# Optimization experiments

Hardware: AMD Instinct MI355X
Metric: run time of the kernel (lower is better)

## Reference

```python
import jax, jax.numpy as jnp
import numpy as np

NUM_LAYERS = 6
DIM = 512
VOCAB = 50257
HEADS = 8
EXPERTS = 8
TOPK = 2
LN_EPS = 1e-5


def setup_inputs() -> dict:
    key = jax.random.key(0)
    ks = jax.random.split(key, 9)
    d, L, E = DIM, NUM_LAYERS, EXPERTS
    return {
        'input_ids': jax.random.randint(ks[0], (2, 1024), 0, VOCAB),
        'embed': jax.random.normal(ks[1], (VOCAB, d), dtype=jnp.float32) * 0.02,
        'qkv_w': jax.random.normal(ks[2], (L, 3 * d, d), dtype=jnp.float32) * 0.02,
        'out_w': jax.random.normal(ks[3], (L, d, d), dtype=jnp.float32) * 0.02,
        'router_w': jax.random.normal(ks[4], (L, E, d), dtype=jnp.float32) * 0.02,
        'router_b': jnp.zeros((L, E), dtype=jnp.float32),
        'w1': jax.random.normal(ks[5], (L, E, 2 * d, d), dtype=jnp.float32) * 0.02,
        'b1': jnp.zeros((L, E, 2 * d), dtype=jnp.float32),
        'w2': jax.random.normal(ks[6], (L, E, d, 2 * d), dtype=jnp.float32) * 0.02,
        'b2': jnp.zeros((L, E, d), dtype=jnp.float32),
        'ln_g': jnp.ones((L, d), dtype=jnp.float32),
        'ln_b': jnp.zeros((L, d), dtype=jnp.float32),
        'head_w': jax.random.normal(ks[7], (VOCAB, d), dtype=jnp.float32) * 0.02,
    }


def _bit_weight(w):
    # BitNet 1.58b training-mode effective weight (STE forward value):
    # scale = mean|w| per output row; w_eff = round(w/scale).clip(-1,1) * scale
    scale = jnp.clip(jnp.mean(jnp.abs(w), axis=-1, keepdims=True), 1e-5, None)
    wq = jnp.clip(jnp.round(w / scale), -1.0, 1.0)
    w_ste = jax.lax.stop_gradient(wq - w) + w
    return w_ste * scale


def _layer_norm(x, g, b):
    mu = jnp.mean(x, axis=-1, keepdims=True)
    var = jnp.mean(jnp.square(x - mu), axis=-1, keepdims=True)
    return (x - mu) * jax.lax.rsqrt(var + LN_EPS) * g + b


def _attention(x, qkv_w, out_w):
    B, Lq, D = x.shape
    hd = D // HEADS
    qkv = (x @ qkv_w.T).reshape(B, Lq, 3, HEADS, hd).transpose(2, 0, 3, 1, 4)
    q, k, v = qkv[0], qkv[1], qkv[2]  # [B,H,L,hd]
    attn = jax.nn.softmax(jnp.einsum('bhqd,bhkd->bhqk', q, k) * hd ** -0.5, axis=-1)
    o = jnp.einsum('bhqk,bhkd->bhqd', attn, v).transpose(0, 2, 1, 3).reshape(B, Lq, D)
    return o @ out_w.T


def _moe(x, rw, rb, w1, b1, w2, b2, g, beta):
    B, Lq, D = x.shape
    N = B * Lq
    xf = x.reshape(N, D)
    probs = jax.nn.softmax(xf @ rw.T + rb, axis=-1)  # [N,E]
    vals, idx = jax.lax.top_k(probs, TOPK)
    vals = vals / (jnp.sum(vals, axis=-1, keepdims=True) + 1e-8)
    # combine weights: [N,E] (top-k indices are distinct, so sum == scatter)
    cw = jnp.sum(jax.nn.one_hot(idx, EXPERTS, dtype=xf.dtype) * vals[..., None], axis=1)
    we1 = _bit_weight(w1)  # [E,2D,D]
    we2 = _bit_weight(w2)  # [E,D,2D]
    h = jax.nn.gelu(jnp.einsum('nd,efd->enf', xf, we1) + b1[:, None, :], approximate=False)
    y = jnp.einsum('enf,edf->end', h, we2) + b2[:, None, :]  # [E,N,D]
    out = jnp.einsum('ne,end->nd', cw, y)
    return _layer_norm(out + xf, g, beta).reshape(B, Lq, D)


def reference(input_ids, embed, qkv_w, out_w, router_w, router_b, w1, b1, w2, b2, ln_g, ln_b, head_w):
    x = embed[input_ids]  # [B,L,D]
    for l in range(NUM_LAYERS):
        x = x + _attention(x, qkv_w[l], out_w[l])
        x = _moe(x, router_w[l], router_b[l], w1[l], b1[l], w2[l], b2[l], ln_g[l], ln_b[l])
    return x @ head_w.T  # logits [B,L,V]
```

## Files before the change

### kernel.cpp

```cpp
#include <hip/hip_runtime.h>
#include <math.h>
#include <stdint.h>

#define NLAYER 6
#define DIMD 512
#define HEADS 8
#define HD 64
#define EXPERTS 8
#define SEQ 1024
#define NTOK 2048
#define FF 1024
#define VOCABN 50257
#define HROWS 50432

typedef __bf16 bf16;
typedef __bf16 bf16x8 __attribute__((ext_vector_type(8)));
typedef __bf16 bf16x4 __attribute__((ext_vector_type(4)));
typedef float f32x4 __attribute__((ext_vector_type(4)));

__device__ __forceinline__ void gl_lds16(const void* g, void* l) {
  __builtin_amdgcn_global_load_lds(
      (const __attribute__((address_space(1))) void*)(uintptr_t)g,
      (__attribute__((address_space(3))) void*)(uintptr_t)l, 16, 0, 0);
}

#define LDSW(row, kg) (((row) * 32) + ((((kg) ^ (((row) >> 1) & 3))) << 3))

__global__ __launch_bounds__(256) void k_mfma_gemm(
    const bf16* __restrict__ A0, const bf16* __restrict__ A1,
    const bf16* __restrict__ B0, const bf16* __restrict__ B1,
    float* __restrict__ Cf, bf16* __restrict__ Cb0, bf16* __restrict__ Cb1,
    bf16* __restrict__ Cb2, bf16* __restrict__ E0, bf16* __restrict__ E1,
    bf16* __restrict__ E2, int M, int N, int K,
    long sA, long sB, long sCf, long sCb,
    const float* __restrict__ colScale, int csStride,
    const float* __restrict__ bias, int biasStride,
    const float* __restrict__ residual, int act, int mode,
    const int* __restrict__ mLimit, const int* __restrict__ aperm,
    int outmode) {
  __shared__ __align__(16) bf16 As[2][128 * 32];
  __shared__ __align__(16) bf16 Bs[2][128 * 32];
  int tid = threadIdx.x;
  int z = blockIdx.z;
  int nwg = gridDim.x * gridDim.y;
  int flat = blockIdx.y * gridDim.x + blockIdx.x;
  int qq = nwg >> 3, rr = nwg & 7;
  int xcd = flat & 7, ii = flat >> 3;
  int swz = (xcd < rr ? xcd * (qq + 1) : rr * (qq + 1) + (xcd - rr) * qq) + ii;
  int m0 = (swz % gridDim.x) * 128, n0 = (swz / gridDim.x) * 128;
  if (mLimit && m0 >= mLimit[z]) return;
  int w = tid >> 6, lane = tid & 63;
  int wm = (w >> 1) * 64, wn = (w & 1) * 64;
  int r15 = lane & 15, kg = lane >> 4;

  int pa[3] = {0, 0, 0}, pb[3] = {0, 0, 0};
  int np = 1;
  if (mode == 3) {
    np = 2; pa[1] = 1;
  } else if (mode == 5) {
    np = 3;
    pa[1] = 0; pb[1] = 1; pa[2] = 1; pb[2] = 0;
  }

  f32x4 acc[4][4] = {};
  int srow = tid >> 2;
  int scol = (((tid & 3) ^ ((tid >> 3) & 3))) << 3;
  long arow0, arow1;
  if (aperm) {
    arow0 = aperm[z * 2048 + m0 + srow];
    arow1 = aperm[z * 2048 + m0 + 64 + srow];
  } else {
    arow0 = m0 + srow;
    arow1 = m0 + 64 + srow;
  }
  const bf16* PA[2] = {A0, A1};
  const bf16* PB[2] = {B0, B1};

  const int kIters = K / 32;
  const int nIter = np * kIters;
  int sp = 0, staged = 0;
  const bf16 *sa0, *sa1, *sb0, *sb1;
  auto resetPassPtrs = [&](int p) {
    const bf16* Az = PA[pa[p]] + (long)z * sA;
    const bf16* Bz = PB[pb[p]] + (long)z * sB;
    sa0 = Az + arow0 * K + scol;
    sa1 = Az + arow1 * K + scol;
    sb0 = Bz + (long)(n0 + srow) * K + scol;
    sb1 = Bz + (long)(n0 + 64 + srow) * K + scol;
  };
  resetPassPtrs(0);
  auto stage = [&](int buf) {
    gl_lds16(sa0, &As[buf][tid * 8]);
    gl_lds16(sa1, &As[buf][2048 + tid * 8]);
    gl_lds16(sb0, &Bs[buf][tid * 8]);
    gl_lds16(sb1, &Bs[buf][2048 + tid * 8]);
    sa0 += 32; sa1 += 32; sb0 += 32; sb1 += 32;
    if (++staged == kIters) {
      staged = 0;
      if (++sp < np) resetPassPtrs(sp);
    }
  };
  auto compute = [&](int buf) {
    bf16x8 af[4], bfr[4];
#pragma unroll
    for (int mi = 0; mi < 4; ++mi) {
      int rowA = wm + mi * 16 + r15;
      af[mi] = *(const bf16x8*)&As[buf][LDSW(rowA, kg)];
    }
#pragma unroll
    for (int ni = 0; ni < 4; ++ni) {
      int rowB = wn + ni * 16 + r15;
      bfr[ni] = *(const bf16x8*)&Bs[buf][LDSW(rowB, kg)];
    }
#pragma unroll
    for (int mi = 0; mi < 4; ++mi)
#pragma unroll
      for (int ni = 0; ni < 4; ++ni)
        acc[mi][ni] = __builtin_amdgcn_mfma_f32_16x16x32_bf16(
            af[mi], bfr[ni], acc[mi][ni], 0, 0, 0);
  };

  stage(0);
  stage(1);
#pragma unroll 1
  for (int it = 0; it < nIter - 2; ++it) {
    asm volatile("s_waitcnt vmcnt(4)" ::: "memory");
    __builtin_amdgcn_s_barrier();
    __builtin_amdgcn_sched_barrier(0);
    compute(it & 1);
    __builtin_amdgcn_s_barrier();
    stage(it & 1);
  }
  asm volatile("s_waitcnt vmcnt(4)" ::: "memory");
  __builtin_amdgcn_s_barrier();
  __builtin_amdgcn_sched_barrier(0);
  compute(nIter & 1);
  asm volatile("s_waitcnt vmcnt(0)" ::: "memory");
  __builtin_amdgcn_s_barrier();
  __builtin_amdgcn_sched_barrier(0);
  compute((nIter - 1) & 1);

#pragma unroll
  for (int mi = 0; mi < 4; ++mi) {
    int rbase = m0 + wm + mi * 16 + kg * 4;
#pragma unroll
    for (int ni = 0; ni < 4; ++ni) {
      int col = n0 + wn + ni * 16 + r15;
      if (col >= N) continue;
      float scl = colScale ? colScale[z * csStride + col] : 1.f;
      float bv = bias ? bias[z * biasStride + col] : 0.f;
#pragma unroll
      for (int reg = 0; reg < 4; ++reg) {
        int row = rbase + reg;
        float v = acc[mi][ni][reg] * scl + bv;
        if (act) v = 0.5f * v * (1.f + erff(v * 0.70710678118654752f));
        if (residual) v += residual[(long)row * N + col];
        if (outmode == 2) {
          int b = row >> 10, qt = row & 1023;
          if (n0 < 512) {
            float qv = v * 0.125f;
            int h = col >> 6, d = col & 63;
            long dst = ((long)(b * 8 + h)) * ((long)SEQ * HD) +
                       (long)qt * HD + d;
            bf16 h0 = (bf16)qv;
            Cb0[dst] = h0;
            Cb1[dst] = (bf16)(qv - (float)h0);
          } else if (n0 < 1024) {
            int c2 = col - 512;
            int h = c2 >> 6, d = c2 & 63;
            long dst = ((long)(b * 8 + h)) * ((long)SEQ * HD) +
                       (long)qt * HD + d;
            bf16 h0 = (bf16)v;
            Cb2[dst] = h0;
            E0[dst] = (bf16)(v - (float)h0);
          } else {
            int c2 = col - 1024;
            int h = c2 >> 6, d = c2 & 63;
            long dst = ((long)(b * 8 + h)) * ((long)HD * SEQ) +
                       (long)d * SEQ + qt;
            bf16 h0 = (bf16)v;
            E1[dst] = h0;
            E2[dst] = (bf16)(v - (float)h0);
          }
          continue;
        }
        if (Cf) Cf[z * sCf + (long)row * N + col] = v;
        if (Cb0) {
          long cib = z * sCb + (long)row * N + col;
          bf16 h0 = (bf16)v;
          Cb0[cib] = h0;
          if (Cb1) {
            float r = v - (float)h0;
            Cb1[cib] = (bf16)r;
          }
        }
      }
    }
  }
}

__global__ __launch_bounds__(256) void k_fattn(
    const bf16* __restrict__ q0b, const bf16* __restrict__ q1b,
    const bf16* __restrict__ k0b, const bf16* __restrict__ k1b,
    const bf16* __restrict__ vt0, const bf16* __restrict__ vt1,
    bf16* __restrict__ at0, bf16* __restrict__ at1) {
  __shared__ __align__(16) bf16 Ks[2][64 * 64];
  __shared__ __align__(16) bf16 Vs[2][64 * 64];
  __shared__ __align__(16) bf16 Ps[2][64 * 64];
  int tid = threadIdx.x;
  int bh = blockIdx.y;
  int q0 = blockIdx.x * 64;
  int w = tid >> 6, lane = tid & 63;
  int r15 = lane & 15, kg = lane >> 4;
  const long bhQK = (long)bh * SEQ * HD;
  const long bhV = (long)bh * HD * SEQ;

  bf16x8 qa0[2], qa1[2];
  {
    long qoff = bhQK + (long)(q0 + w * 16 + r15) * HD;
#pragma unroll
    for (int ks = 0; ks < 2; ++ks) {
      qa0[ks] = *(const bf16x8*)&q0b[qoff + ks * 32 + kg * 8];
      qa1[ks] = *(const bf16x8*)&q1b[qoff + ks * 32 + kg * 8];
    }
  }

  auto stageK = [&](int kt) {
#pragma unroll
    for (int i = 0; i < 2; ++i) {
      int L = tid + i * 256;
      int row = L >> 3, pc = L & 7;
      int gc = pc ^ (row & 7);
      long gsrc = bhQK + (long)(kt * 64 + row) * HD + gc * 8;
      gl_lds16(k0b + gsrc, &Ks[0][L * 8]);
      gl_lds16(k1b + gsrc, &Ks[1][L * 8]);
    }
  };
  auto stageV = [&](int kt) {
#pragma unroll
    for (int i = 0; i < 2; ++i) {
      int L = tid + i * 256;
      int row = L >> 3, pc = L & 7;
      int gc = pc ^ (row & 7);
      long gsrc = bhV + (long)row * SEQ + kt * 64 + gc * 8;
      gl_lds16(vt0 + gsrc, &Vs[0][L * 8]);
      gl_lds16(vt1 + gsrc, &Vs[1][L * 8]);
    }
  };
  auto computeS = [&](f32x4* sf) {
    __builtin_amdgcn_s_setprio(1);
#pragma unroll
    for (int kc = 0; kc < 4; ++kc) {
      f32x4 a = {};
      int rowB = kc * 16 + r15;
#pragma unroll
      for (int ks = 0; ks < 2; ++ks) {
        int pc = (ks * 4 + kg) ^ (rowB & 7);
        bf16x8 b0 = *(const bf16x8*)&Ks[0][rowB * 64 + pc * 8];
        bf16x8 b1 = *(const bf16x8*)&Ks[1][rowB * 64 + pc * 8];
        a = __builtin_amdgcn_mfma_f32_16x16x32_bf16(qa0[ks], b0, a, 0, 0, 0);
        a = __builtin_amdgcn_mfma_f32_16x16x32_bf16(qa0[ks], b1, a, 0, 0, 0);
        a = __builtin_amdgcn_mfma_f32_16x16x32_bf16(qa1[ks], b0, a, 0, 0, 0);
      }
      sf[kc] = a;
    }
    __builtin_amdgcn_s_setprio(0);
  };

  float m[4], l[4];
#pragma unroll
  for (int r = 0; r < 4; ++r) { m[r] = -1e30f; l[r] = 0.f; }
  f32x4 oacc[4] = {};

  for (int kt = 0; kt < SEQ / 64; ++kt) {
    stageK(kt);
    stageV(kt);
    __syncthreads();
    f32x4 sf[4];
    computeS(sf);
#pragma unroll
    for (int r = 0; r < 4; ++r) {
      float tm = sf[0][r];
#pragma unroll
      for (int kc = 1; kc < 4; ++kc) tm = fmaxf(tm, sf[kc][r]);
      tm = fmaxf(tm, __shfl_xor(tm, 1));
      tm = fmaxf(tm, __shfl_xor(tm, 2));
      tm = fmaxf(tm, __shfl_xor(tm, 4));
      tm = fmaxf(tm, __shfl_xor(tm, 8));
      float mn = fmaxf(m[r], tm);
      float corr = __expf(m[r] - mn);
      float s = 0.f;
#pragma unroll
      for (int kc = 0; kc < 4; ++kc) {
        float p = __expf(sf[kc][r] - mn);
        sf[kc][r] = p;
        s += p;
      }
      s += __shfl_xor(s, 1);
      s += __shfl_xor(s, 2);
      s += __shfl_xor(s, 4);
      s += __shfl_xor(s, 8);
      l[r] = l[r] * corr + s;
      m[r] = mn;
#pragma unroll
      for (int dg = 0; dg < 4; ++dg) oacc[dg][r] *= corr;
    }
#pragma unroll
    for (int kc = 0; kc < 4; ++kc) {
#pragma unroll
      for (int r = 0; r < 4; ++r) {
        float p = sf[kc][r];
        bf16 h0 = (bf16)p;
        bf16 h1 = (bf16)(p - (float)h0);
        int qrow = w * 16 + kg * 4 + r;
        int kcol = kc * 16 + r15;
        int pc = (kcol >> 3) ^ (qrow & 7);
        int addr = qrow * 64 + pc * 8 + (kcol & 7);
        Ps[0][addr] = h0;
        Ps[1][addr] = h1;
      }
    }
    bf16x8 pa0[2], pa1[2];
    int rowP = w * 16 + r15;
#pragma unroll
    for (int ks = 0; ks < 2; ++ks) {
      int pc = (ks * 4 + kg) ^ (rowP & 7);
      pa0[ks] = *(const bf16x8*)&Ps[0][rowP * 64 + pc * 8];
      pa1[ks] = *(const bf16x8*)&Ps[1][rowP * 64 + pc * 8];
    }
    __builtin_amdgcn_s_setprio(1);
#pragma unroll
    for (int dg = 0; dg < 4; ++dg) {
      int rowV = dg * 16 + r15;
#pragma unroll
      for (int ks = 0; ks < 2; ++ks) {
        int pc = (ks * 4 + kg) ^ (rowV & 7);
        bf16x8 v0 = *(const bf16x8*)&Vs[0][rowV * 64 + pc * 8];
        bf16x8 v1 = *(const bf16x8*)&Vs[1][rowV * 64 + pc * 8];
        oacc[dg] = __builtin_amdgcn_mfma_f32_16x16x32_bf16(pa0[ks], v0,
                                                           oacc[dg], 0, 0, 0);
        oacc[dg] = __builtin_amdgcn_mfma_f32_16x16x32_bf16(pa0[ks], v1,
                                                           oacc[dg], 0, 0, 0);
        oacc[dg] = __builtin_amdgcn_mfma_f32_16x16x32_bf16(pa1[ks], v0,
                                                           oacc[dg], 0, 0, 0);
      }
    }
    __builtin_amdgcn_s_setprio(0);
    __syncthreads();
  }

  float invl[4];
#pragma unroll
  for (int r = 0; r < 4; ++r) invl[r] = 1.f / l[r];

  int b = bh >> 3, h = bh & 7;
#pragma unroll
  for (int dg = 0; dg < 4; ++dg) {
#pragma unroll
    for (int r = 0; r < 4; ++r) {
      int qrow = q0 + w * 16 + kg * 4 + r;
      int d = dg * 16 + r15;
      long dst = ((long)(b * SEQ + qrow)) * DIMD + h * HD + d;
      float v = oacc[dg][r] * invl[r];
      bf16 h0 = (bf16)v;
      at0[dst] = h0;
      at1[dst] = (bf16)(v - (float)h0);
    }
  }
}

__global__ __launch_bounds__(512, 2) void k_hgemm(const bf16* __restrict__ A,
                                                  const bf16* __restrict__ Bt,
                                                  float* __restrict__ C,
                                                  int M, int N, int K) {
  __shared__ __align__(16) bf16 As[2][256 * 64];
  __shared__ __align__(16) bf16 Bs[2][256 * 64];
  int tid = threadIdx.x;
  int nwg = gridDim.x * gridDim.y;
  int flat = blockIdx.y * gridDim.x + blockIdx.x;
  int qq = nwg >> 3, rr = nwg & 7;
  int xcd = flat & 7, ii = flat >> 3;
  int swz = (xcd < rr ? xcd * (qq + 1) : rr * (qq + 1) + (xcd - rr) * qq) + ii;
  int m0 = (swz % gridDim.x) * 256, n0 = (swz / gridDim.x) * 256;
  int w = tid >> 6, lane = tid & 63;
  int wm = (w >> 2) * 128, wn = (w & 3) * 64;
  int r15 = lane & 15, kg = lane >> 4;

  auto stage = [&](int buf, int kt) {
#pragma unroll
    for (int j = 0; j < 4; ++j) {
      int L = tid + j * 512;
      int row = L >> 3, pc = L & 7;
      int gc = pc ^ (row & 7);
      gl_lds16(A + (long)(m0 + row) * K + kt * 64 + gc * 8, &As[buf][L * 8]);
      gl_lds16(Bt + (long)(n0 + row) * K + kt * 64 + gc * 8, &Bs[buf][L * 8]);
    }
  };

  f32x4 acc[8][4] = {};
  auto compute = [&](int buf) {
#pragma unroll
    for (int ks = 0; ks < 2; ++ks) {
      bf16x8 af[8], bf_[4];
#pragma unroll
      for (int mi = 0; mi < 8; ++mi) {
        int row = wm + mi * 16 + r15;
        af[mi] = *(const bf16x8*)
            &As[buf][row * 64 + ((((ks * 4 + kg) ^ (row & 7))) << 3)];
      }
#pragma unroll
      for (int ni = 0; ni < 4; ++ni) {
        int row = wn + ni * 16 + r15;
        bf_[ni] = *(const bf16x8*)
            &Bs[buf][row * 64 + ((((ks * 4 + kg) ^ (row & 7))) << 3)];
      }
#pragma unroll
      for (int mi = 0; mi < 8; ++mi)
#pragma unroll
        for (int ni = 0; ni < 4; ++ni)
          acc[mi][ni] = __builtin_amdgcn_mfma_f32_16x16x32_bf16(
              af[mi], bf_[ni], acc[mi][ni], 0, 0, 0);
    }
  };

  stage(0, 0);
  stage(1, 1);
#pragma unroll 1
  for (int t = 0; t < 6; ++t) {
    asm volatile("s_waitcnt vmcnt(8)" ::: "memory");
    __builtin_amdgcn_s_barrier();
    __builtin_amdgcn_sched_barrier(0);
    compute(t & 1);
    __builtin_amdgcn_s_barrier();
    stage(t & 1, t + 2);
  }
  asm volatile("s_waitcnt vmcnt(8)" ::: "memory");
  __builtin_amdgcn_s_barrier();
  __builtin_amdgcn_sched_barrier(0);
  compute(0);
  asm volatile("s_waitcnt vmcnt(0)" ::: "memory");
  __builtin_amdgcn_s_barrier();
  __builtin_amdgcn_sched_barrier(0);
  compute(1);

#pragma unroll
  for (int mi = 0; mi < 8; ++mi) {
    int rbase = m0 + wm + mi * 16 + kg * 4;
#pragma unroll
    for (int ni = 0; ni < 4; ++ni) {
      int col = n0 + wn + ni * 16 + r15;
      if (col >= N) continue;
#pragma unroll
      for (int reg = 0; reg < 4; ++reg)
        C[(long)(rbase + reg) * N + col] = acc[mi][ni][reg];
    }
  }
}

__global__ __launch_bounds__(256) void k_embed(const int* __restrict__ ids,
                                               const float* __restrict__ E,
                                               float* __restrict__ xf,
                                               bf16* __restrict__ x0,
                                               bf16* __restrict__ x1) {
  int i = blockIdx.x * 256 + threadIdx.x;
  if (i >= NTOK * DIMD) return;
  int n = i >> 9, d = i & 511;
  float v = E[(long)ids[n] * DIMD + d];
  xf[i] = v;
  bf16 b0 = (bf16)v;
  x0[i] = b0;
  x1[i] = (bf16)(v - (float)b0);
}

__global__ __launch_bounds__(256) void k_prepw(const float* __restrict__ qkv_w,
                                               const float* __restrict__ out_w,
                                               bf16* __restrict__ qw0a,
                                               bf16* __restrict__ qw1a,
                                               bf16* __restrict__ ow0a,
                                               bf16* __restrict__ ow1a) {
  int l = blockIdx.y;
  const long n8q = (long)3 * DIMD * DIMD / 8;
  long i = (long)blockIdx.x * 256 + threadIdx.x;
  const float* s;
  bf16 *d0, *d1;
  long j;
  if (i < n8q) {
    s = qkv_w + (long)l * 3 * DIMD * DIMD;
    d0 = qw0a + (long)l * 3 * DIMD * DIMD;
    d1 = qw1a + (long)l * 3 * DIMD * DIMD;
    j = i;
  } else {
    s = out_w + (long)l * DIMD * DIMD;
    d0 = ow0a + (long)l * DIMD * DIMD;
    d1 = ow1a + (long)l * DIMD * DIMD;
    j = i - n8q;
  }
  const float4* s4 = (const float4*)s;
  float4 a = s4[2 * j], b = s4[2 * j + 1];
  float vv[8] = {a.x, a.y, a.z, a.w, b.x, b.y, b.z, b.w};
  bf16x8 o0, o1;
#pragma unroll
  for (int k = 0; k < 8; ++k) {
    float v = vv[k];
    bf16 h0 = (bf16)v;
    o0[k] = h0;
    o1[k] = (bf16)(v - (float)h0);
  }
  ((bf16x8*)d0)[j] = o0;
  ((bf16x8*)d1)[j] = o1;
}

__global__ __launch_bounds__(256) void k_headconv(const float* __restrict__ s,
                                                  bf16* __restrict__ d) {
  long i = (long)blockIdx.x * 256 + threadIdx.x;
  long n8 = (long)HROWS * DIMD / 8;
  if (i >= n8) return;
  long row = i / (DIMD / 8);
  bf16x8 o;
  if (row < VOCABN) {
    const float4* s4 = (const float4*)s;
    float4 a = s4[2 * i], b = s4[2 * i + 1];
    o[0] = (bf16)a.x; o[1] = (bf16)a.y; o[2] = (bf16)a.z; o[3] = (bf16)a.w;
    o[4] = (bf16)b.x; o[5] = (bf16)b.y; o[6] = (bf16)b.z; o[7] = (bf16)b.w;
  } else {
    o = (bf16x8)(bf16)0.f;
  }
  ((bf16x8*)d)[i] = o;
}

__global__ __launch_bounds__(64) void k_router(const float* __restrict__ x,
                                               const float* __restrict__ rw,
                                               const float* __restrict__ rb,
                                               int* __restrict__ top2,
                                               float* __restrict__ v2) {
  int n = blockIdx.x;
  int t = threadIdx.x;
  int e = t >> 3, part = t & 7;
  __shared__ float red[64];
  const float* xr = x + (long)n * DIMD;
  const float* wr = rw + (long)e * DIMD;
  float d = 0.f;
  int c0 = part * 64;
#pragma unroll
  for (int c = 0; c < 64; c += 4) {
    float4 xv = *(const float4*)(xr + c0 + c);
    float4 wv = *(const float4*)(wr + c0 + c);
    d += xv.x * wv.x + xv.y * wv.y + xv.z * wv.z + xv.w * wv.w;
  }
  red[t] = d;
  __syncthreads();
  if (t < 8) {
    float logit = rb[t];
    for (int pp = 0; pp < 8; ++pp) logit += red[t * 8 + pp];
    red[t] = logit;
  }
  __syncthreads();
  if (t == 0) {
    float p2[8];
    float m = -1e30f;
    for (int i = 0; i < 8; ++i) m = fmaxf(m, red[i]);
    float s = 0.f;
    for (int i = 0; i < 8; ++i) { p2[i] = expf(red[i] - m); s += p2[i]; }
    for (int i = 0; i < 8; ++i) p2[i] /= s;
    int i1 = 0;
    for (int i = 1; i < 8; ++i) if (p2[i] > p2[i1]) i1 = i;
    int i2 = (i1 == 0) ? 1 : 0;
    for (int i = 0; i < 8; ++i) {
      if (i == i1 || i == i2) continue;
      if (p2[i] > p2[i2]) i2 = i;
    }
    float sum = p2[i1] + p2[i2] + 1e-8f;
    top2[2 * n] = i1;
    top2[2 * n + 1] = i2;
    v2[2 * n] = p2[i1] / sum;
    v2[2 * n + 1] = p2[i2] / sum;
  }
}

__global__ __launch_bounds__(256) void k_expcnt(const int* __restrict__ top2,
                                                int* __restrict__ perm,
                                                int* __restrict__ tokpos,
                                                int* __restrict__ cnt,
                                                bf16* __restrict__ zx0,
                                                bf16* __restrict__ zx1) {
  int e = blockIdx.x, t = threadIdx.x;
  if (e == 0) {
    for (int c = t; c < DIMD; c += 256) {
      zx0[c] = (bf16)0.f;
      zx1[c] = (bf16)0.f;
    }
  }
  __shared__ int sc[256];
  int fl[8];
  int f = 0;
#pragma unroll
  for (int j = 0; j < 8; ++j) {
    int n = t * 8 + j;
    int m = (top2[2 * n] == e || top2[2 * n + 1] == e) ? 1 : 0;
    fl[j] = m;
    f += m;
  }
  sc[t] = f;
  __syncthreads();
  for (int o = 1; o < 256; o <<= 1) {
    int v = (t >= o) ? sc[t - o] : 0;
    __syncthreads();
    sc[t] += v;
    __syncthreads();
  }
  int pos = sc[t] - f;
#pragma unroll
  for (int j = 0; j < 8; ++j) {
    if (fl[j]) {
      int n = t * 8 + j;
      perm[e * 2048 + pos] = n;
      int jj = (top2[2 * n] == e) ? 0 : 1;
      tokpos[2 * n + jj] = e * 2048 + pos;
      ++pos;
    }
  }
  int total = sc[255];
  int cpad = (total + 127) & ~127;
  for (int i = total + t; i < cpad; i += 256) perm[e * 2048 + i] = 2048;
  if (t == 0) cnt[e] = total;
}

__global__ __launch_bounds__(256) void k_bitw2(const float* __restrict__ w1,
                                               const float* __restrict__ w2,
                                               bf16* __restrict__ we1qa,
                                               float* __restrict__ s1a,
                                               bf16* __restrict__ we2qa,
                                               float* __restrict__ s2a) {
  int l = blockIdx.y;
  int blk = blockIdx.x;
  int t = threadIdx.x;
  const float* wr;
  bf16* outr;
  float* sOut;
  int cols;
  if (blk < EXPERTS * FF) {
    cols = DIMD;
    wr = w1 + (long)l * EXPERTS * FF * DIMD + (long)blk * cols;
    outr = we1qa + (long)l * EXPERTS * FF * DIMD + (long)blk * cols;
    sOut = s1a + (long)l * EXPERTS * FF + blk;
  } else {
    int row = blk - EXPERTS * FF;
    cols = FF;
    wr = w2 + (long)l * EXPERTS * DIMD * FF + (long)row * cols;
    outr = we2qa + (long)l * EXPERTS * DIMD * FF + (long)row * cols;
    sOut = s2a + (long)l * EXPERTS * DIMD + row;
  }
  float acc = 0.f;
  for (int c = t; c < cols; c += 256) acc += fabsf(wr[c]);
  __shared__ float red[256];
  red[t] = acc;
  __syncthreads();
  for (int off = 128; off; off >>= 1) {
    if (t < off) red[t] += red[t + off];
    __syncthreads();
  }
  float scale = fmaxf(red[0] / (float)cols, 1e-5f);
  if (t == 0) *sOut = scale;
  for (int c = t; c < cols; c += 256) {
    float qv = rintf(wr[c] / scale);
    qv = fmaxf(-1.f, fminf(1.f, qv));
    outr[c] = (bf16)qv;
  }
}

__global__ __launch_bounds__(128) void k_lncomb(
    const float* __restrict__ yg, const int* __restrict__ tokpos,
    const float* __restrict__ v2, const float* __restrict__ xBf,
    const float* __restrict__ g, const float* __restrict__ b,
    float* __restrict__ xof, bf16* __restrict__ x0, bf16* __restrict__ x1) {
  int n = blockIdx.x;
  int t = threadIdx.x;
  __shared__ float red[128];
  long tp0 = tokpos[2 * n], tp1 = tokpos[2 * n + 1];
  float w0 = v2[2 * n], w1 = v2[2 * n + 1];
  const float* y0 = yg + tp0 * DIMD;
  const float* y1 = yg + tp1 * DIMD;
  float u[4];
  float s = 0.f;
#pragma unroll
  for (int i = 0; i < 4; ++i) {
    int d = t + i * 128;
    float v = xBf[(long)n * DIMD + d] + w0 * y0[d] + w1 * y1[d];
    u[i] = v;
    s += v;
  }
  red[t] = s;
  __syncthreads();
  for (int off = 64; off; off >>= 1) {
    if (t < off) red[t] += red[t + off];
    __syncthreads();
  }
  float mu = red[0] / (float)DIMD;
  __syncthreads();
  float var = 0.f;
#pragma unroll
  for (int i = 0; i < 4; ++i) {
    float d = u[i] - mu;
    var += d * d;
  }
  red[t] = var;
  __syncthreads();
  for (int off = 64; off; off >>= 1) {
    if (t < off) red[t] += red[t + off];
    __syncthreads();
  }
  float inv = 1.f / sqrtf(red[0] / (float)DIMD + 1e-5f);
#pragma unroll
  for (int i = 0; i < 4; ++i) {
    int c = t + i * 128;
    float v = (u[i] - mu) * inv * g[c] + b[c];
    long oi = (long)n * DIMD + c;
    xof[oi] = v;
    bf16 b0 = (bf16)v;
    x0[oi] = b0;
    x1[oi] = (bf16)(v - (float)b0);
  }
}

extern "C" void kernel_launch(void* const* d_in, const int* in_sizes, int n_in,
                              void* d_out, int out_size, void* d_ws, size_t ws_size,
                              hipStream_t stream) {
  const int* ids = (const int*)d_in[0];
  const float* embed = (const float*)d_in[1];
  const float* qkv_w = (const float*)d_in[2];
  const float* out_w = (const float*)d_in[3];
  const float* router_w = (const float*)d_in[4];
  const float* router_b = (const float*)d_in[5];
  const float* w1 = (const float*)d_in[6];
  const float* b1 = (const float*)d_in[7];
  const float* w2 = (const float*)d_in[8];
  const float* b2 = (const float*)d_in[9];
  const float* ln_g = (const float*)d_in[10];
  const float* ln_b = (const float*)d_in[11];
  const float* head_w = (const float*)d_in[12];
  float* out = (float*)d_out;

  char* base = (char*)d_ws;
  size_t off = 0;
  auto alloc = [&](size_t bytes) -> void* {
    void* p = base + off;
    off += (bytes + 255) & ~(size_t)255;
    return p;
  };
  const size_t ND = (size_t)NTOK * DIMD;
  float* xAf = (float*)alloc(ND * 4);
  float* xBf = (float*)alloc(ND * 4);
  int* top2 = (int*)alloc((size_t)NTOK * 2 * 4);
  float* v2 = (float*)alloc((size_t)NTOK * 2 * 4);
  int* perm = (int*)alloc((size_t)EXPERTS * 2048 * 4);
  int* tokpos = (int*)alloc((size_t)NTOK * 2 * 4);
  int* cntb = (int*)alloc(64);
  bf16* xA0 = (bf16*)alloc(ND * 2);
  bf16* xA1 = (bf16*)alloc(ND * 2);
  bf16* xB0 = (bf16*)alloc((ND + DIMD) * 2);
  bf16* xB1 = (bf16*)alloc((ND + DIMD) * 2);
  bf16* at0 = (bf16*)alloc(ND * 2);
  bf16* at1 = (bf16*)alloc(ND * 2);
  bf16* q0b = (bf16*)alloc((size_t)16 * SEQ * HD * 2);
  bf16* q1b = (bf16*)alloc((size_t)16 * SEQ * HD * 2);
  bf16* k0b = (bf16*)alloc((size_t)16 * SEQ * HD * 2);
  bf16* k1b = (bf16*)alloc((size_t)16 * SEQ * HD * 2);
  bf16* vt0b = (bf16*)alloc((size_t)16 * HD * SEQ * 2);
  bf16* vt1b = (bf16*)alloc((size_t)16 * HD * SEQ * 2);
  bf16* qw0a = (bf16*)alloc((size_t)NLAYER * 3 * DIMD * DIMD * 2);
  bf16* qw1a = (bf16*)alloc((size_t)NLAYER * 3 * DIMD * DIMD * 2);
  bf16* ow0a = (bf16*)alloc((size_t)NLAYER * DIMD * DIMD * 2);
  bf16* ow1a = (bf16*)alloc((size_t)NLAYER * DIMD * DIMD * 2);
  bf16* we1qa = (bf16*)alloc((size_t)NLAYER * EXPERTS * FF * DIMD * 2);
  float* s1a = (float*)alloc((size_t)NLAYER * EXPERTS * FF * 4);
  bf16* we2qa = (bf16*)alloc((size_t)NLAYER * EXPERTS * DIMD * FF * 2);
  float* s2a = (float*)alloc((size_t)NLAYER * EXPERTS * DIMD * 4);

  size_t Ustart = off;
  bf16* h0g = (bf16*)alloc((size_t)EXPERTS * 2048 * FF * 2);
  bf16* h1g = (bf16*)alloc((size_t)EXPERTS * 2048 * FF * 2);
  float* yg = (float*)alloc((size_t)EXPERTS * 2048 * DIMD * 4);
  size_t endB = off;
  size_t endC = Ustart + (size_t)HROWS * DIMD * 2;
  bf16* hw0 = (bf16*)(base + Ustart);
  off = endB > endC ? endB : endC;
  if (ws_size < off) return;

  k_embed<<<(NTOK * DIMD + 255) / 256, 256, 0, stream>>>(ids, embed, xAf, xA0,
                                                         xA1);
  k_prepw<<<dim3(512, NLAYER), 256, 0, stream>>>(qkv_w, out_w, qw0a, qw1a,
                                                 ow0a, ow1a);
  k_bitw2<<<dim3(EXPERTS * FF + EXPERTS * DIMD, NLAYER), 256, 0, stream>>>(
      w1, w2, we1qa, s1a, we2qa, s2a);

  for (int l = 0; l < NLAYER; ++l) {
    bf16* qw0 = qw0a + (long)l * 3 * DIMD * DIMD;
    bf16* qw1 = qw1a + (long)l * 3 * DIMD * DIMD;
    bf16* ow0 = ow0a + (long)l * DIMD * DIMD;
    bf16* ow1 = ow1a + (long)l * DIMD * DIMD;
    bf16* we1q = we1qa + (long)l * EXPERTS * FF * DIMD;
    bf16* we2q = we2qa + (long)l * EXPERTS * DIMD * FF;
    float* s1 = s1a + (long)l * EXPERTS * FF;
    float* s2 = s2a + (long)l * EXPERTS * DIMD;
    k_mfma_gemm<<<dim3(NTOK / 128, (3 * DIMD) / 128, 1), 256, 0, stream>>>(
        xA0, xA1, qw0, qw1, nullptr, q0b, q1b, k0b, k1b, vt0b, vt1b,
        NTOK, 3 * DIMD, DIMD, 0, 0, 0, 0,
        nullptr, 0, nullptr, 0, nullptr, 0, 5, nullptr, nullptr, 2);
    k_fattn<<<dim3(SEQ / 64, 16), 256, 0, stream>>>(q0b, q1b, k0b, k1b,
                                                    vt0b, vt1b, at0, at1);
    k_mfma_gemm<<<dim3(NTOK / 128, DIMD / 128, 1), 256, 0, stream>>>(
        at0, at1, ow0, ow1, xBf, xB0, xB1, nullptr, nullptr, nullptr,
        nullptr, NTOK, DIMD, DIMD, 0, 0, 0, 0,
        nullptr, 0, nullptr, 0, xAf, 0, 5, nullptr, nullptr, 0);
    k_router<<<NTOK, 64, 0, stream>>>(xBf, router_w + (long)l * EXPERTS * DIMD,
                                      router_b + l * EXPERTS, top2, v2);
    k_expcnt<<<EXPERTS, 256, 0, stream>>>(top2, perm, tokpos, cntb,
                                          xB0 + ND, xB1 + ND);
    k_mfma_gemm<<<dim3(NTOK / 128, FF / 128, EXPERTS), 256, 0, stream>>>(
        xB0, xB1, we1q, nullptr, nullptr, h0g, h1g, nullptr, nullptr, nullptr,
        nullptr, NTOK, FF, DIMD, 0, (long)FF * DIMD, 0, (long)2048 * FF,
        s1, FF, b1 + (long)l * EXPERTS * FF, FF, nullptr, 1, 3, cntb, perm, 0);
    k_mfma_gemm<<<dim3(NTOK / 128, DIMD / 128, EXPERTS), 256, 0, stream>>>(
        h0g, h1g, we2q, nullptr, yg, nullptr, nullptr, nullptr, nullptr,
        nullptr, nullptr, NTOK, DIMD, FF, (long)2048 * FF, (long)DIMD * FF,
        (long)2048 * DIMD, 0, s2, DIMD, b2 + (long)l * EXPERTS * DIMD, DIMD,
        nullptr, 0, 3, cntb, nullptr, 0);
    k_lncomb<<<NTOK, 128, 0, stream>>>(yg, tokpos, v2, xBf, ln_g + l * DIMD,
                                       ln_b + l * DIMD, xAf, xA0, xA1);
  }
  long nh8 = (long)HROWS * DIMD / 8;
  k_headconv<<<(int)((nh8 + 255) / 256), 256, 0, stream>>>(head_w, hw0);
  k_hgemm<<<dim3(NTOK / 256, HROWS / 256, 1), 512, 0, stream>>>(
      xA0, hw0, out, NTOK, VOCABN, DIMD);
}
```

Before: 2.002 ms.

## Triple-buffer GEMM LDS tiles and double-buffer K/V prefetch in flash attention

```diff
diff --git a/kernel.cpp b/kernel.cpp
--- a/kernel.cpp
+++ b/kernel.cpp
@@ -38,8 +38,8 @@
     const float* __restrict__ residual, int act, int mode,
     const int* __restrict__ mLimit, const int* __restrict__ aperm,
     int outmode) {
-  __shared__ __align__(16) bf16 As[2][128 * 32];
-  __shared__ __align__(16) bf16 Bs[2][128 * 32];
+  __shared__ __align__(16) bf16 As[3][128 * 32];
+  __shared__ __align__(16) bf16 Bs[3][128 * 32];
   int tid = threadIdx.x;
   int z = blockIdx.z;
   int nwg = gridDim.x * gridDim.y;
@@ -122,23 +122,32 @@
 
   stage(0);
   stage(1);
+  stage(2);
+  int buf = 0;
 #pragma unroll 1
-  for (int it = 0; it < nIter - 2; ++it) {
-    asm volatile("s_waitcnt vmcnt(4)" ::: "memory");
+  for (int it = 0; it < nIter - 3; ++it) {
+    asm volatile("s_waitcnt vmcnt(8)" ::: "memory");
     __builtin_amdgcn_s_barrier();
     __builtin_amdgcn_sched_barrier(0);
-    compute(it & 1);
+    compute(buf);
     __builtin_amdgcn_s_barrier();
-    stage(it & 1);
-  }
+    stage(buf);
+    buf = (buf == 2) ? 0 : buf + 1;
+  }
+  asm volatile("s_waitcnt vmcnt(8)" ::: "memory");
+  __builtin_amdgcn_s_barrier();
+  __builtin_amdgcn_sched_barrier(0);
+  compute(buf);
+  buf = (buf == 2) ? 0 : buf + 1;
   asm volatile("s_waitcnt vmcnt(4)" ::: "memory");
   __builtin_amdgcn_s_barrier();
   __builtin_amdgcn_sched_barrier(0);
-  compute(nIter & 1);
+  compute(buf);
+  buf = (buf == 2) ? 0 : buf + 1;
   asm volatile("s_waitcnt vmcnt(0)" ::: "memory");
   __builtin_amdgcn_s_barrier();
   __builtin_amdgcn_sched_barrier(0);
-  compute((nIter - 1) & 1);
+  compute(buf);
 
 #pragma unroll
   for (int mi = 0; mi < 4; ++mi) {
@@ -204,8 +213,8 @@
     const bf16* __restrict__ k0b, const bf16* __restrict__ k1b,
     const bf16* __restrict__ vt0, const bf16* __restrict__ vt1,
     bf16* __restrict__ at0, bf16* __restrict__ at1) {
-  __shared__ __align__(16) bf16 Ks[2][64 * 64];
-  __shared__ __align__(16) bf16 Vs[2][64 * 64];
+  __shared__ __align__(16) bf16 Ks[2][2][64 * 64];
+  __shared__ __align__(16) bf16 Vs[2][2][64 * 64];
   __shared__ __align__(16) bf16 Ps[2][64 * 64];
   int tid = threadIdx.x;
   int bh = blockIdx.y;
@@ -225,29 +234,28 @@
     }
   }
 
-  auto stageK = [&](int kt) {
+  float m[4], l[4];
+#pragma unroll
+  for (int r = 0; r < 4; ++r) { m[r] = -1e30f; l[r] = 0.f; }
+  f32x4 oacc[4] = {};
+
+  auto stageKV = [&](int buf, int kt) {
 #pragma unroll
     for (int i = 0; i < 2; ++i) {
       int L = tid + i * 256;
       int row = L >> 3, pc = L & 7;
       int gc = pc ^ (row & 7);
-      long gsrc = bhQK + (long)(kt * 64 + row) * HD + gc * 8;
-      gl_lds16(k0b + gsrc, &Ks[0][L * 8]);
-      gl_lds16(k1b + gsrc, &Ks[1][L * 8]);
+      long gK = bhQK + (long)(kt * 64 + row) * HD + gc * 8;
+      gl_lds16(k0b + gK, &Ks[buf][0][L * 8]);
+      gl_lds16(k1b + gK, &Ks[buf][1][L * 8]);
+      long gV = bhV + (long)row * SEQ + kt * 64 + gc * 8;
+      gl_lds16(vt0 + gV, &Vs[buf][0][L * 8]);
+      gl_lds16(vt1 + gV, &Vs[buf][1][L * 8]);
     }
   };
-  auto stageV = [&](int kt) {
-#pragma unroll
-    for (int i = 0; i < 2; ++i) {
-      int L = tid + i * 256;
-      int row = L >> 3, pc = L & 7;
-      int gc = pc ^ (row & 7);
-      long gsrc = bhV + (long)row * SEQ + kt * 64 + gc * 8;
-      gl_lds16(vt0 + gsrc, &Vs[0][L * 8]);
-      gl_lds16(vt1 + gsrc, &Vs[1][L * 8]);
-    }
-  };
-  auto computeS = [&](f32x4* sf) {
+
+  auto computeTile = [&](int buf) {
+    f32x4 sf[4];
     __builtin_amdgcn_s_setprio(1);
 #pragma unroll
     for (int kc = 0; kc < 4; ++kc) {
@@ -256,8 +264,8 @@
 #pragma unroll
       for (int ks = 0; ks < 2; ++ks) {
         int pc = (ks * 4 + kg) ^ (rowB & 7);
-        bf16x8 b0 = *(const bf16x8*)&Ks[0][rowB * 64 + pc * 8];
-        bf16x8 b1 = *(const bf16x8*)&Ks[1][rowB * 64 + pc * 8];
+        bf16x8 b0 = *(const bf16x8*)&Ks[buf][0][rowB * 64 + pc * 8];
+        bf16x8 b1 = *(const bf16x8*)&Ks[buf][1][rowB * 64 + pc * 8];
         a = __builtin_amdgcn_mfma_f32_16x16x32_bf16(qa0[ks], b0, a, 0, 0, 0);
         a = __builtin_amdgcn_mfma_f32_16x16x32_bf16(qa0[ks], b1, a, 0, 0, 0);
         a = __builtin_amdgcn_mfma_f32_16x16x32_bf16(qa1[ks], b0, a, 0, 0, 0);
@@ -265,19 +273,6 @@
       sf[kc] = a;
     }
     __builtin_amdgcn_s_setprio(0);
-  };
-
-  float m[4], l[4];
-#pragma unroll
-  for (int r = 0; r < 4; ++r) { m[r] = -1e30f; l[r] = 0.f; }
-  f32x4 oacc[4] = {};
-
-  for (int kt = 0; kt < SEQ / 64; ++kt) {
-    stageK(kt);
-    stageV(kt);
-    __syncthreads();
-    f32x4 sf[4];
-    computeS(sf);
 #pragma unroll
     for (int r = 0; r < 4; ++r) {
       float tm = sf[0][r];
@@ -335,8 +330,8 @@
 #pragma unroll
       for (int ks = 0; ks < 2; ++ks) {
         int pc = (ks * 4 + kg) ^ (rowV & 7);
-        bf16x8 v0 = *(const bf16x8*)&Vs[0][rowV * 64 + pc * 8];
-        bf16x8 v1 = *(const bf16x8*)&Vs[1][rowV * 64 + pc * 8];
+        bf16x8 v0 = *(const bf16x8*)&Vs[buf][0][rowV * 64 + pc * 8];
+        bf16x8 v1 = *(const bf16x8*)&Vs[buf][1][rowV * 64 + pc * 8];
         oacc[dg] = __builtin_amdgcn_mfma_f32_16x16x32_bf16(pa0[ks], v0,
                                                            oacc[dg], 0, 0, 0);
         oacc[dg] = __builtin_amdgcn_mfma_f32_16x16x32_bf16(pa0[ks], v1,
@@ -346,8 +341,27 @@
       }
     }
     __builtin_amdgcn_s_setprio(0);
-    __syncthreads();
-  }
+  };
+
+  stageKV(0, 0);
+  stageKV(1, 1);
+#pragma unroll 1
+  for (int kt = 0; kt < SEQ / 64 - 2; ++kt) {
+    asm volatile("s_waitcnt vmcnt(8)" ::: "memory");
+    __builtin_amdgcn_s_barrier();
+    __builtin_amdgcn_sched_barrier(0);
+    computeTile(kt & 1);
+    __builtin_amdgcn_s_barrier();
+    stageKV(kt & 1, kt + 2);
+  }
+  asm volatile("s_waitcnt vmcnt(8)" ::: "memory");
+  __builtin_amdgcn_s_barrier();
+  __builtin_amdgcn_sched_barrier(0);
+  computeTile(0);
+  asm volatile("s_waitcnt vmcnt(0)" ::: "memory");
+  __builtin_amdgcn_s_barrier();
+  __builtin_amdgcn_sched_barrier(0);
+  computeTile(1);
 
   float invl[4];
 #pragma unroll
```

Result: slower. 2.334 ms (+16.6%).

## Template GEMM to stage split-bf16 operand halves together in one K loop

Applied to the files above, without the earlier changes.

```diff
diff --git a/kernel.cpp b/kernel.cpp
--- a/kernel.cpp
+++ b/kernel.cpp
@@ -26,7 +26,8 @@
 
 #define LDSW(row, kg) (((row) * 32) + ((((kg) ^ (((row) >> 1) & 3))) << 3))
 
-__global__ __launch_bounds__(256) void k_mfma_gemm(
+template <int NA, int NB>
+__global__ __launch_bounds__(256) void k_gemm(
     const bf16* __restrict__ A0, const bf16* __restrict__ A1,
     const bf16* __restrict__ B0, const bf16* __restrict__ B1,
     float* __restrict__ Cf, bf16* __restrict__ Cb0, bf16* __restrict__ Cb1,
@@ -35,11 +36,11 @@
     long sA, long sB, long sCf, long sCb,
     const float* __restrict__ colScale, int csStride,
     const float* __restrict__ bias, int biasStride,
-    const float* __restrict__ residual, int act, int mode,
+    const float* __restrict__ residual, int act,
     const int* __restrict__ mLimit, const int* __restrict__ aperm,
     int outmode) {
-  __shared__ __align__(16) bf16 As[2][128 * 32];
-  __shared__ __align__(16) bf16 Bs[2][128 * 32];
+  __shared__ __align__(16) bf16 As[2][NA][128 * 32];
+  __shared__ __align__(16) bf16 Bs[2][NB][128 * 32];
   int tid = threadIdx.x;
   int z = blockIdx.z;
   int nwg = gridDim.x * gridDim.y;
@@ -53,15 +54,6 @@
   int wm = (w >> 1) * 64, wn = (w & 1) * 64;
   int r15 = lane & 15, kg = lane >> 4;
 
-  int pa[3] = {0, 0, 0}, pb[3] = {0, 0, 0};
-  int np = 1;
-  if (mode == 3) {
-    np = 2; pa[1] = 1;
-  } else if (mode == 5) {
-    np = 3;
-    pa[1] = 0; pb[1] = 1; pa[2] = 1; pb[2] = 0;
-  }
-
   f32x4 acc[4][4] = {};
   int srow = tid >> 2;
   int scol = (((tid & 3) ^ ((tid >> 3) & 3))) << 3;
@@ -75,70 +67,94 @@
   }
   const bf16* PA[2] = {A0, A1};
   const bf16* PB[2] = {B0, B1};
-
-  const int kIters = K / 32;
-  const int nIter = np * kIters;
-  int sp = 0, staged = 0;
-  const bf16 *sa0, *sa1, *sb0, *sb1;
-  auto resetPassPtrs = [&](int p) {
-    const bf16* Az = PA[pa[p]] + (long)z * sA;
-    const bf16* Bz = PB[pb[p]] + (long)z * sB;
-    sa0 = Az + arow0 * K + scol;
-    sa1 = Az + arow1 * K + scol;
-    sb0 = Bz + (long)(n0 + srow) * K + scol;
-    sb1 = Bz + (long)(n0 + 64 + srow) * K + scol;
-  };
-  resetPassPtrs(0);
+  const bf16* aP[NA][2];
+  const bf16* bP[NB][2];
+#pragma unroll
+  for (int a = 0; a < NA; ++a) {
+    const bf16* Az = PA[a] + (long)z * sA;
+    aP[a][0] = Az + arow0 * K + scol;
+    aP[a][1] = Az + arow1 * K + scol;
+  }
+#pragma unroll
+  for (int b = 0; b < NB; ++b) {
+    const bf16* Bz = PB[b] + (long)z * sB;
+    bP[b][0] = Bz + (long)(n0 + srow) * K + scol;
+    bP[b][1] = Bz + (long)(n0 + 64 + srow) * K + scol;
+  }
+
   auto stage = [&](int buf) {
-    gl_lds16(sa0, &As[buf][tid * 8]);
-    gl_lds16(sa1, &As[buf][2048 + tid * 8]);
-    gl_lds16(sb0, &Bs[buf][tid * 8]);
-    gl_lds16(sb1, &Bs[buf][2048 + tid * 8]);
-    sa0 += 32; sa1 += 32; sb0 += 32; sb1 += 32;
-    if (++staged == kIters) {
-      staged = 0;
-      if (++sp < np) resetPassPtrs(sp);
+#pragma unroll
+    for (int a = 0; a < NA; ++a) {
+      gl_lds16(aP[a][0], &As[buf][a][tid * 8]);
+      gl_lds16(aP[a][1], &As[buf][a][2048 + tid * 8]);
+      aP[a][0] += 32;
+      aP[a][1] += 32;
+    }
+#pragma unroll
+    for (int b = 0; b < NB; ++b) {
+      gl_lds16(bP[b][0], &Bs[buf][b][tid * 8]);
+      gl_lds16(bP[b][1], &Bs[buf][b][2048 + tid * 8]);
+      bP[b][0] += 32;
+      bP[b][1] += 32;
     }
   };
   auto compute = [&](int buf) {
-    bf16x8 af[4], bfr[4];
-#pragma unroll
-    for (int mi = 0; mi < 4; ++mi) {
-      int rowA = wm + mi * 16 + r15;
-      af[mi] = *(const bf16x8*)&As[buf][LDSW(rowA, kg)];
-    }
-#pragma unroll
-    for (int ni = 0; ni < 4; ++ni) {
-      int rowB = wn + ni * 16 + r15;
-      bfr[ni] = *(const bf16x8*)&Bs[buf][LDSW(rowB, kg)];
-    }
-#pragma unroll
-    for (int mi = 0; mi < 4; ++mi)
-#pragma unroll
-      for (int ni = 0; ni < 4; ++ni)
-        acc[mi][ni] = __builtin_amdgcn_mfma_f32_16x16x32_bf16(
-            af[mi], bfr[ni], acc[mi][ni], 0, 0, 0);
+    bf16x8 af[NA][4], bfr[NB][4];
+#pragma unroll
+    for (int a = 0; a < NA; ++a)
+#pragma unroll
+      for (int mi = 0; mi < 4; ++mi) {
+        int rowA = wm + mi * 16 + r15;
+        af[a][mi] = *(const bf16x8*)&As[buf][a][LDSW(rowA, kg)];
+      }
+#pragma unroll
+    for (int b = 0; b < NB; ++b)
+#pragma unroll
+      for (int ni = 0; ni < 4; ++ni) {
+        int rowB = wn + ni * 16 + r15;
+        bfr[b][ni] = *(const bf16x8*)&Bs[buf][b][LDSW(rowB, kg)];
+      }
+#pragma unroll
+    for (int a = 0; a < NA; ++a)
+#pragma unroll
+      for (int b = 0; b < NB; ++b) {
+        if (a + b <= 1) {
+#pragma unroll
+          for (int mi = 0; mi < 4; ++mi)
+#pragma unroll
+            for (int ni = 0; ni < 4; ++ni)
+              acc[mi][ni] = __builtin_amdgcn_mfma_f32_16x16x32_bf16(
+                  af[a][mi], bfr[b][ni], acc[mi][ni], 0, 0, 0);
+        }
+      }
   };
-
+  auto waitStage = [&]() {
+    if constexpr (NA + NB == 4)
+      asm volatile("s_waitcnt vmcnt(8)" ::: "memory");
+    else
+      asm volatile("s_waitcnt vmcnt(6)" ::: "memory");
+  };
+
+  const int kIters = K / 32;
   stage(0);
   stage(1);
 #pragma unroll 1
-  for (int it = 0; it < nIter - 2; ++it) {
-    asm volatile("s_waitcnt vmcnt(4)" ::: "memory");
+  for (int it = 0; it < kIters - 2; ++it) {
+    waitStage();
     __builtin_amdgcn_s_barrier();
     __builtin_amdgcn_sched_barrier(0);
     compute(it & 1);
     __builtin_amdgcn_s_barrier();
     stage(it & 1);
   }
-  asm volatile("s_waitcnt vmcnt(4)" ::: "memory");
+  waitStage();
   __builtin_amdgcn_s_barrier();
   __builtin_amdgcn_sched_barrier(0);
-  compute(nIter & 1);
+  compute(kIters & 1);
   asm volatile("s_waitcnt vmcnt(0)" ::: "memory");
   __builtin_amdgcn_s_barrier();
   __builtin_amdgcn_sched_barrier(0);
-  compute((nIter - 1) & 1);
+  compute((kIters - 1) & 1);
 
 #pragma unroll
   for (int mi = 0; mi < 4; ++mi) {
@@ -802,29 +818,29 @@
     bf16* we2q = we2qa + (long)l * EXPERTS * DIMD * FF;
     float* s1 = s1a + (long)l * EXPERTS * FF;
     float* s2 = s2a + (long)l * EXPERTS * DIMD;
-    k_mfma_gemm<<<dim3(NTOK / 128, (3 * DIMD) / 128, 1), 256, 0, stream>>>(
+    k_gemm<2, 2><<<dim3(NTOK / 128, (3 * DIMD) / 128, 1), 256, 0, stream>>>(
         xA0, xA1, qw0, qw1, nullptr, q0b, q1b, k0b, k1b, vt0b, vt1b,
         NTOK, 3 * DIMD, DIMD, 0, 0, 0, 0,
-        nullptr, 0, nullptr, 0, nullptr, 0, 5, nullptr, nullptr, 2);
+        nullptr, 0, nullptr, 0, nullptr, 0, nullptr, nullptr, 2);
     k_fattn<<<dim3(SEQ / 64, 16), 256, 0, stream>>>(q0b, q1b, k0b, k1b,
                                                     vt0b, vt1b, at0, at1);
-    k_mfma_gemm<<<dim3(NTOK / 128, DIMD / 128, 1), 256, 0, stream>>>(
+    k_gemm<2, 2><<<dim3(NTOK / 128, DIMD / 128, 1), 256, 0, stream>>>(
         at0, at1, ow0, ow1, xBf, xB0, xB1, nullptr, nullptr, nullptr,
         nullptr, NTOK, DIMD, DIMD, 0, 0, 0, 0,
-        nullptr, 0, nullptr, 0, xAf, 0, 5, nullptr, nullptr, 0);
+        nullptr, 0, nullptr, 0, xAf, 0, nullptr, nullptr, 0);
     k_router<<<NTOK, 64, 0, stream>>>(xBf, router_w + (long)l * EXPERTS * DIMD,
                                       router_b + l * EXPERTS, top2, v2);
     k_expcnt<<<EXPERTS, 256, 0, stream>>>(top2, perm, tokpos, cntb,
                                           xB0 + ND, xB1 + ND);
-    k_mfma_gemm<<<dim3(NTOK / 128, FF / 128, EXPERTS), 256, 0, stream>>>(
+    k_gemm<2, 1><<<dim3(NTOK / 128, FF / 128, EXPERTS), 256, 0, stream>>>(
         xB0, xB1, we1q, nullptr, nullptr, h0g, h1g, nullptr, nullptr, nullptr,
         nullptr, NTOK, FF, DIMD, 0, (long)FF * DIMD, 0, (long)2048 * FF,
-        s1, FF, b1 + (long)l * EXPERTS * FF, FF, nullptr, 1, 3, cntb, perm, 0);
-    k_mfma_gemm<<<dim3(NTOK / 128, DIMD / 128, EXPERTS), 256, 0, stream>>>(
+        s1, FF, b1 + (long)l * EXPERTS * FF, FF, nullptr, 1, cntb, perm, 0);
+    k_gemm<2, 1><<<dim3(NTOK / 128, DIMD / 128, EXPERTS), 256, 0, stream>>>(
         h0g, h1g, we2q, nullptr, yg, nullptr, nullptr, nullptr, nullptr,
         nullptr, nullptr, NTOK, DIMD, FF, (long)2048 * FF, (long)DIMD * FF,
         (long)2048 * DIMD, 0, s2, DIMD, b2 + (long)l * EXPERTS * DIMD, DIMD,
-        nullptr, 0, 3, cntb, nullptr, 0);
+        nullptr, 0, cntb, nullptr, 0);
     k_lncomb<<<NTOK, 128, 0, stream>>>(yg, tokpos, v2, xBf, ln_g + l * DIMD,
                                        ln_b + l * DIMD, xAf, xA0, xA1);
   }
```

Measured after the change: 2.713 ms. 1.36x slower.
